# Kernel tuning notes

Measured on AMD Instinct MI355X. Metric: run time of the kernel, lower is better.

## Reference

```python
import jax, jax.numpy as jnp
import numpy as np

jax.config.update("jax_enable_x64", True)  # torch uses double for the scale decomposition

ACC = 23  # 'accuracy' in integer_multiply_shift_round


def _fixed_point_mul(x_int, new_scale):
    """Bit-exact integer multiply-shift-round: x * new_scale where
    new_scale = m * 2**e (frexp), m quantized to ACC-bit integer mantissa."""
    m, e = jnp.frexp(new_scale)                      # m in [0.5, 1)
    nm = jnp.round(m * (1 << ACC)).astype(jnp.int64)  # torch casts to int32 (ACC<32); int64 is a safe superset
    tmp = x_int.astype(jnp.int64) * nm                # [B,S,D] int64
    e = e.astype(jnp.int64)
    sl = jnp.maximum(e - ACC, 0)                      # left-shift amount (e - ACC >= 0 branch)
    sr = jnp.maximum(ACC - e, 0)                      # right-shift amount (sr_round_na branch)
    left = tmp << sl
    bit = (tmp < 0).astype(jnp.int64)
    nudge = (jnp.int64(1) << jnp.maximum(sr - 1, 0)) - bit   # round-half-away-from-zero nudge
    right = jnp.where(sr > 0, (tmp + nudge) >> sr, tmp)      # sr==0 -> identity (sr_round_na early return)
    return jnp.where(e - ACC >= 0, left, right)


def setup_inputs() -> dict:
    key = jax.random.key(0)
    k1, k2 = jax.random.split(key)
    B, S, D = 4, 4096, 2048
    # integer-valued pre-activations (int32 accumulators), stored as float32 holding exact ints
    x = jax.random.randint(k1, (B, S, D), -2048, 2048, dtype=jnp.int32).astype(jnp.float32)
    identity = jax.random.randint(k2, (B, S, D), -2048, 2048, dtype=jnp.int32).astype(jnp.float32)
    return {
        "x": x,
        "identity": identity,
        "pre_act_scaling_factor": jnp.array([0.004], jnp.float32),
        "identity_scaling_factor": jnp.array([0.002], jnp.float32),
        "x_min": jnp.array([-8.0], jnp.float32),   # calibrated activation range buffers
        "x_max": jnp.array([8.0], jnp.float32),
    }


def reference(x, identity, pre_act_scaling_factor, identity_scaling_factor, x_min, x_max):
    bit = 8
    n = 2 ** (bit - 1) - 1  # 127
    # symmetric_linear_quantization_params (per-tensor)
    scale = jnp.clip(jnp.maximum(jnp.abs(x_min), jnp.abs(x_max)), 1e-8, None) / n  # [1] float32
    # FixedPointMul: requantize pre_act and identity to the output scale, add, clamp
    s64 = scale.astype(jnp.float64)
    ns_x = pre_act_scaling_factor.astype(jnp.float64) / s64
    ns_id = identity_scaling_factor.astype(jnp.float64) / s64
    out = _fixed_point_mul(x.astype(jnp.int64), ns_x) + _fixed_point_mul(identity.astype(jnp.int64), ns_id)
    q = jnp.clip(out, -n - 1, n).astype(jnp.int8)  # bit_num<=8 -> int8
    # QuantAct returns dequantized activation and its scale
    return q.astype(jnp.float32) * scale.astype(jnp.float32), scale
```

## Files before the change

kernel.cpp:

```cpp
#include <hip/hip_runtime.h>
#include <math.h>

#define ACC_BITS 23

typedef float f32x4 __attribute__((ext_vector_type(4)));

#define TPB   256
#define VPT   4
#define TILE  (TPB * VPT)

struct QP {
    float scale;
    int   fast;
    int   nmx_hi, nmx_lo, Kx, srx12;
    int   nmi_hi, nmi_lo, Ki, sri12;
    long long nm_x64, nm_i64;
    int   e_x, e_i;
};

__device__ __forceinline__ QP compute_qparams(float pre, float idsf,
                                              float xmn, float xmx) {
    QP q;
    float s     = fmaxf(fmaxf(fabsf(xmn), fabsf(xmx)), 1e-8f);
    float scale = s / 127.0f;

    double s64  = (double)scale;
    double ns_x = (double)pre  / s64;
    double ns_i = (double)idsf / s64;

    int e_x, e_i;
    double m_x = frexp(ns_x, &e_x);
    double m_i = frexp(ns_i, &e_i);
    long long nm_x = (long long)rint(m_x * 8388608.0);
    long long nm_i = (long long)rint(m_i * 8388608.0);

    q.scale  = scale;
    q.nm_x64 = nm_x;  q.e_x = e_x;
    q.nm_i64 = nm_i;  q.e_i = e_i;

    long long ax = nm_x, ai = nm_i;
    int ex = e_x, ei = e_i;
    if (ax == (1LL << 23)) { ax >>= 1; ex += 1; }
    if (ai == (1LL << 23)) { ai >>= 1; ei += 1; }
    int sr_x = ACC_BITS - ex, sr_i = ACC_BITS - ei;

    q.fast = (ax > 0) && (ax < (1LL << 23)) &&
             (ai > 0) && (ai < (1LL << 23)) &&
             (sr_x >= 12) && (sr_x <= 30) && (sr_i >= 12) && (sr_i <= 30);
    q.nmx_hi = (int)(ax >> 12); q.nmx_lo = (int)(ax & 0xFFF);
    q.nmi_hi = (int)(ai >> 12); q.nmi_lo = (int)(ai & 0xFFF);
    q.Kx = q.fast ? (1 << (sr_x - 1)) : 0;
    q.Ki = q.fast ? (1 << (sr_i - 1)) : 0;
    q.srx12 = sr_x - 12;
    q.sri12 = sr_i - 12;
    return q;
}

__device__ __forceinline__ long long fixed_point_mul64(long long xi, long long nm, int e) {
    long long tmp = xi * nm;
    if (e - ACC_BITS >= 0) {
        return tmp << (e - ACC_BITS);
    } else {
        int sr = ACC_BITS - e;
        long long nudge = (1LL << (sr - 1)) - (long long)(tmp < 0);
        return (tmp + nudge) >> sr;
    }
}

__device__ __forceinline__ int fpm24(int xi, int nm_hi, int nm_lo, int K, int sr12) {
    int bit = (int)((unsigned)xi >> 31);
    int B = (__mul24(xi, nm_lo) + K - bit) >> 12;
    int A = __mul24(xi, nm_hi);
    return (A + B) >> sr12;
}

__global__ void __launch_bounds__(TPB)
quantact_fused(const f32x4* __restrict__ x,
               const f32x4* __restrict__ idn,
               f32x4* __restrict__ out,
               float* __restrict__ out_scale,
               const float* __restrict__ pre_sf,
               const float* __restrict__ id_sf,
               const float* __restrict__ xminp,
               const float* __restrict__ xmaxp,
               int n4, int n)
{
    const int base = blockIdx.x * TILE + (int)threadIdx.x;
    const bool full = (base + (VPT - 1) * TPB) < n4;

    const float pre  = pre_sf[0];
    const float idsf = id_sf[0];
    const float xmn  = xminp[0];
    const float xmx  = xmaxp[0];

    f32x4 xv[VPT], iv[VPT];
    if (full) {
        #pragma unroll
        for (int k = 0; k < VPT; ++k) {
            xv[k] = x  [base + k * TPB];
            iv[k] = idn[base + k * TPB];
        }
    }
    __builtin_amdgcn_sched_barrier(0);

    const QP q = compute_qparams(pre, idsf, xmn, xmx);
    const float scale = q.scale;

    if (blockIdx.x == 0 && threadIdx.x == 0) *out_scale = scale;

    if (q.fast) {
        const int nmx_hi = q.nmx_hi, nmx_lo = q.nmx_lo, Kx = q.Kx, srx = q.srx12;
        const int nmi_hi = q.nmi_hi, nmi_lo = q.nmi_lo, Ki = q.Ki, sri = q.sri12;

        if (full) {
            #pragma unroll
            for (int k = 0; k < VPT; ++k) {
                f32x4 ov;
                #pragma unroll
                for (int c = 0; c < 4; ++c) {
                    int o = fpm24((int)xv[k][c], nmx_hi, nmx_lo, Kx, srx)
                          + fpm24((int)iv[k][c], nmi_hi, nmi_lo, Ki, sri);
                    o = o < -128 ? -128 : (o > 127 ? 127 : o);
                    ov[c] = (float)o * scale;
                }
                out[base + k * TPB] = ov;
            }
        } else {
            #pragma unroll
            for (int k = 0; k < VPT; ++k) {
                int i = base + k * TPB;
                if (i < n4) {
                    f32x4 xw = x[i], iw = idn[i], ov;
                    #pragma unroll
                    for (int c = 0; c < 4; ++c) {
                        int o = fpm24((int)xw[c], nmx_hi, nmx_lo, Kx, srx)
                              + fpm24((int)iw[c], nmi_hi, nmi_lo, Ki, sri);
                        o = o < -128 ? -128 : (o > 127 ? 127 : o);
                        ov[c] = (float)o * scale;
                    }
                    out[i] = ov;
                }
            }
        }
    } else {
        const long long nm64_x = q.nm_x64, nm64_i = q.nm_i64;
        const int e_x = q.e_x, e_i = q.e_i;
        #pragma unroll
        for (int k = 0; k < VPT; ++k) {
            int i = base + k * TPB;
            if (i < n4) {
                f32x4 xw, iw, ov;
                if (full) { xw = xv[k]; iw = iv[k]; }
                else      { xw = x[i];  iw = idn[i]; }
                #pragma unroll
                for (int c = 0; c < 4; ++c) {
                    long long o = fixed_point_mul64((long long)xw[c], nm64_x, e_x)
                                + fixed_point_mul64((long long)iw[c], nm64_i, e_i);
                    o = o < -128 ? -128 : (o > 127 ? 127 : o);
                    ov[c] = (float)(int)o * scale;
                }
                out[i] = ov;
            }
        }
    }

    if (blockIdx.x == 0) {
        const float* xs  = (const float*)x;
        const float* is_ = (const float*)idn;
        float* os = (float*)out;
        const long long nm64_x = q.nm_x64, nm64_i = q.nm_i64;
        const int e_x = q.e_x, e_i = q.e_i;
        for (int j = n4 * 4 + (int)threadIdx.x; j < n; j += TPB) {
            long long o = fixed_point_mul64((long long)xs[j], nm64_x, e_x)
                        + fixed_point_mul64((long long)is_[j], nm64_i, e_i);
            o = o < -128 ? -128 : (o > 127 ? 127 : o);
            os[j] = (float)(int)o * scale;
        }
    }
}

extern "C" void kernel_launch(void* const* d_in, const int* in_sizes, int n_in,
                              void* d_out, int out_size, void* d_ws, size_t ws_size,
                              hipStream_t stream) {
    const f32x4* x      = (const f32x4*)d_in[0];
    const f32x4* idn    = (const f32x4*)d_in[1];
    const float* pre_sf = (const float*)d_in[2];
    const float* id_sf  = (const float*)d_in[3];
    const float* xmin   = (const float*)d_in[4];
    const float* xmax   = (const float*)d_in[5];

    int n  = in_sizes[0];
    int n4 = n / 4;

    float* out       = (float*)d_out;
    float* out_scale = out + n;

    int grid = (n4 + TILE - 1) / TILE;
    if (grid < 1) grid = 1;
    quantact_fused<<<grid, TPB, 0, stream>>>(x, idn, (f32x4*)out, out_scale,
                                             pre_sf, id_sf, xmin, xmax, n4, n);
}
```

Baseline: 315.5 us.

## Use persistent grid-stride blocks with double-buffered register tile prefetch

```diff
diff --git a/kernel.cpp b/kernel.cpp
--- a/kernel.cpp
+++ b/kernel.cpp
@@ -8,6 +8,7 @@
 #define TPB   256
 #define VPT   4
 #define TILE  (TPB * VPT)
+#define NBLK  1024
 
 struct QP {
     float scale;
@@ -74,7 +75,67 @@
     return (A + B) >> sr12;
 }
 
-__global__ void __launch_bounds__(TPB)
+__device__ __forceinline__ void load_tile(const f32x4* __restrict__ x,
+                                          const f32x4* __restrict__ idn,
+                                          int tl, int tid, int n4,
+                                          f32x4 (&xv)[VPT], f32x4 (&iv)[VPT]) {
+    const int b = tl * TILE + tid;
+    if (b + (VPT - 1) * TPB < n4) {
+        #pragma unroll
+        for (int k = 0; k < VPT; ++k) {
+            xv[k] = x  [b + k * TPB];
+            iv[k] = idn[b + k * TPB];
+        }
+    } else {
+        #pragma unroll
+        for (int k = 0; k < VPT; ++k) {
+            int i = b + k * TPB;
+            if (i < n4) { xv[k] = x[i]; iv[k] = idn[i]; }
+            else        { xv[k] = (f32x4)0.f; iv[k] = (f32x4)0.f; }
+        }
+    }
+}
+
+__device__ __forceinline__ void process_tile(const f32x4 (&xv)[VPT],
+                                             const f32x4 (&iv)[VPT],
+                                             f32x4* __restrict__ out,
+                                             int tl, int tid, int n4,
+                                             const QP& q) {
+    const int b = tl * TILE + tid;
+    const float scale = q.scale;
+    if (q.fast && (b + (VPT - 1) * TPB < n4)) {
+        #pragma unroll
+        for (int k = 0; k < VPT; ++k) {
+            f32x4 ov;
+            #pragma unroll
+            for (int c = 0; c < 4; ++c) {
+                int o = fpm24((int)xv[k][c], q.nmx_hi, q.nmx_lo, q.Kx, q.srx12)
+                      + fpm24((int)iv[k][c], q.nmi_hi, q.nmi_lo, q.Ki, q.sri12);
+                o = o < -128 ? -128 : (o > 127 ? 127 : o);
+                ov[c] = (float)o * scale;
+            }
+            out[b + k * TPB] = ov;
+        }
+    } else {
+        #pragma unroll
+        for (int k = 0; k < VPT; ++k) {
+            int i = b + k * TPB;
+            if (i < n4) {
+                f32x4 ov;
+                #pragma unroll
+                for (int c = 0; c < 4; ++c) {
+                    long long o = fixed_point_mul64((long long)xv[k][c], q.nm_x64, q.e_x)
+                                + fixed_point_mul64((long long)iv[k][c], q.nm_i64, q.e_i);
+                    o = o < -128 ? -128 : (o > 127 ? 127 : o);
+                    ov[c] = (float)(int)o * scale;
+                }
+                out[i] = ov;
+            }
+        }
+    }
+}
+
+__global__ void __launch_bounds__(TPB, 4)
 quantact_fused(const f32x4* __restrict__ x,
                const f32x4* __restrict__ idn,
                f32x4* __restrict__ out,
@@ -85,82 +146,39 @@
                const float* __restrict__ xmaxp,
                int n4, int n)
 {
-    const int base = blockIdx.x * TILE + (int)threadIdx.x;
-    const bool full = (base + (VPT - 1) * TPB) < n4;
+    const int tid    = (int)threadIdx.x;
+    const int ntiles = (n4 + TILE - 1) / TILE;
+    const int nb     = (int)gridDim.x;
 
     const float pre  = pre_sf[0];
     const float idsf = id_sf[0];
     const float xmn  = xminp[0];
     const float xmx  = xmaxp[0];
 
-    f32x4 xv[VPT], iv[VPT];
-    if (full) {
-        #pragma unroll
-        for (int k = 0; k < VPT; ++k) {
-            xv[k] = x  [base + k * TPB];
-            iv[k] = idn[base + k * TPB];
-        }
-    }
+    int t = (int)blockIdx.x;
+    f32x4 xa[VPT], ia[VPT], xb[VPT], ib[VPT];
+
+    if (t < ntiles) load_tile(x, idn, t, tid, n4, xa, ia);
     __builtin_amdgcn_sched_barrier(0);
 
     const QP q = compute_qparams(pre, idsf, xmn, xmx);
-    const float scale = q.scale;
-
-    if (blockIdx.x == 0 && threadIdx.x == 0) *out_scale = scale;
-
-    if (q.fast) {
-        const int nmx_hi = q.nmx_hi, nmx_lo = q.nmx_lo, Kx = q.Kx, srx = q.srx12;
-        const int nmi_hi = q.nmi_hi, nmi_lo = q.nmi_lo, Ki = q.Ki, sri = q.sri12;
-
-        if (full) {
-            #pragma unroll
-            for (int k = 0; k < VPT; ++k) {
-                f32x4 ov;
-                #pragma unroll
-                for (int c = 0; c < 4; ++c) {
-                    int o = fpm24((int)xv[k][c], nmx_hi, nmx_lo, Kx, srx)
-                          + fpm24((int)iv[k][c], nmi_hi, nmi_lo, Ki, sri);
-                    o = o < -128 ? -128 : (o > 127 ? 127 : o);
-                    ov[c] = (float)o * scale;
-                }
-                out[base + k * TPB] = ov;
-            }
-        } else {
-            #pragma unroll
-            for (int k = 0; k < VPT; ++k) {
-                int i = base + k * TPB;
-                if (i < n4) {
-                    f32x4 xw = x[i], iw = idn[i], ov;
-                    #pragma unroll
-                    for (int c = 0; c < 4; ++c) {
-                        int o = fpm24((int)xw[c], nmx_hi, nmx_lo, Kx, srx)
-                              + fpm24((int)iw[c], nmi_hi, nmi_lo, Ki, sri);
-                        o = o < -128 ? -128 : (o > 127 ? 127 : o);
-                        ov[c] = (float)o * scale;
-                    }
-                    out[i] = ov;
-                }
-            }
-        }
-    } else {
-        const long long nm64_x = q.nm_x64, nm64_i = q.nm_i64;
-        const int e_x = q.e_x, e_i = q.e_i;
-        #pragma unroll
-        for (int k = 0; k < VPT; ++k) {
-            int i = base + k * TPB;
-            if (i < n4) {
-                f32x4 xw, iw, ov;
-                if (full) { xw = xv[k]; iw = iv[k]; }
-                else      { xw = x[i];  iw = idn[i]; }
-                #pragma unroll
-                for (int c = 0; c < 4; ++c) {
-                    long long o = fixed_point_mul64((long long)xw[c], nm64_x, e_x)
-                                + fixed_point_mul64((long long)iw[c], nm64_i, e_i);
-                    o = o < -128 ? -128 : (o > 127 ? 127 : o);
-                    ov[c] = (float)(int)o * scale;
-                }
-                out[i] = ov;
-            }
+    if (blockIdx.x == 0 && tid == 0) *out_scale = q.scale;
+
+    if (t < ntiles) {
+        for (;;) {
+            int t2 = t + nb;
+            if (t2 >= ntiles) { process_tile(xa, ia, out, t, tid, n4, q); break; }
+            load_tile(x, idn, t2, tid, n4, xb, ib);
+            __builtin_amdgcn_sched_barrier(0);
+            process_tile(xa, ia, out, t, tid, n4, q);
+            t = t2;
+
+            int t3 = t + nb;
+            if (t3 >= ntiles) { process_tile(xb, ib, out, t, tid, n4, q); break; }
+            load_tile(x, idn, t3, tid, n4, xa, ia);
+            __builtin_amdgcn_sched_barrier(0);
+            process_tile(xb, ib, out, t, tid, n4, q);
+            t = t3;
         }
     }
 
@@ -168,13 +186,11 @@
         const float* xs  = (const float*)x;
         const float* is_ = (const float*)idn;
         float* os = (float*)out;
-        const long long nm64_x = q.nm_x64, nm64_i = q.nm_i64;
-        const int e_x = q.e_x, e_i = q.e_i;
-        for (int j = n4 * 4 + (int)threadIdx.x; j < n; j += TPB) {
-            long long o = fixed_point_mul64((long long)xs[j], nm64_x, e_x)
-                        + fixed_point_mul64((long long)is_[j], nm64_i, e_i);
+        for (int j = n4 * 4 + tid; j < n; j += TPB) {
+            long long o = fixed_point_mul64((long long)xs[j], q.nm_x64, q.e_x)
+                        + fixed_point_mul64((long long)is_[j], q.nm_i64, q.e_i);
             o = o < -128 ? -128 : (o > 127 ? 127 : o);
-            os[j] = (float)(int)o * scale;
+            os[j] = (float)(int)o * q.scale;
         }
     }
 }
@@ -195,8 +211,8 @@
     float* out       = (float*)d_out;
     float* out_scale = out + n;
 
-    int grid = (n4 + TILE - 1) / TILE;
-    if (grid < 1) grid = 1;
+    int ntiles = (n4 + TILE - 1) / TILE;
+    int grid   = ntiles < NBLK ? (ntiles < 1 ? 1 : ntiles) : NBLK;
     quantact_fused<<<grid, TPB, 0, stream>>>(x, idn, (f32x4*)out, out_scale,
                                              pre_sf, id_sf, xmin, xmax, n4, n);
 }
```

Result: no change. 319.0 us (+1.1%).
